# Performance work log

Measured on AMD Instinct MI355X. Metric: run time of the kernel, lower is better.

## Reference

```python
import jax, jax.numpy as jnp
import numpy as np

D, H = 256, 8
DH = D // H
NH, NL = 1024, 65536
EH, EL = 16384, 262144


def setup_inputs() -> dict:
    key = jax.random.key(0)
    ks = jax.random.split(key, 24)
    w = lambda i, s=0.05: jax.random.normal(ks[i], (D, D), jnp.float32) * s
    z = jnp.zeros((D,), jnp.float32)
    return {
        'high_emb_in': jax.random.normal(ks[0], (NH, D), jnp.float32),
        'low_emb_in': jax.random.normal(ks[1], (NL, D), jnp.float32),
        'high_edge_index': jax.random.randint(ks[2], (2, EH), 0, NH, jnp.int32),
        'low_edge_index': jax.random.randint(ks[3], (2, EL), 0, NL, jnp.int32),
        'low_batch': jnp.sort(jax.random.randint(ks[4], (NL,), 0, NH, jnp.int32)),
        'ln_g': jnp.ones((D,), jnp.float32), 'ln_b': z,
        'gin_eps': jnp.zeros((), jnp.float32), 'gin_w': w(5), 'gin_b': z,
        'mha_wq': w(6), 'mha_bq': z, 'mha_wk': w(7), 'mha_bk': z,
        'mha_wv': w(8), 'mha_bv': z, 'mha_wo': w(9), 'mha_bo': z,
        'tc_wq': w(10), 'tc_bq': z, 'tc_wk': w(11), 'tc_bk': z,
        'tc_wv': w(12), 'tc_bv': z, 'tc_wskip': w(13), 'tc_bskip': z,
        'chl_q': w(14), 'chl_k': w(15), 'chl_v': w(16),
        'clh_q': w(17), 'clh_k': w(18), 'clh_v': w(19),
    }


def _ln(x, g, b):
    m = x.mean(-1, keepdims=True)
    v = ((x - m) ** 2).mean(-1, keepdims=True)
    return (x - m) / jnp.sqrt(v + 1e-5) * g + b


def reference(high_emb_in, low_emb_in, ln_g, ln_b, gin_eps, gin_w, gin_b,
              mha_wq, mha_bq, mha_wk, mha_bk, mha_wv, mha_bv, mha_wo, mha_bo,
              tc_wq, tc_bq, tc_wk, tc_bk, tc_wv, tc_bv, tc_wskip, tc_bskip,
              chl_q, chl_k, chl_v, clh_q, clh_k, clh_v,
              high_edge_index, low_edge_index, low_batch):
    he = _ln(high_emb_in, ln_g, ln_b)
    le = _ln(low_emb_in, ln_g, ln_b)

    # --- GINConv(Linear) on high graph: Linear((1+eps)*x + sum_{j->i} x_j) ---
    hs, hd = high_edge_index[0], high_edge_index[1]
    agg = jax.ops.segment_sum(he[hs], hd, num_segments=NH)
    gin = ((1.0 + gin_eps) * he + agg) @ gin_w + gin_b

    # --- MultiheadAttention (unbatched self-attention over high nodes) ---
    q = (he @ mha_wq + mha_bq).reshape(NH, H, DH)
    k = (he @ mha_wk + mha_bk).reshape(NH, H, DH)
    v = (he @ mha_wv + mha_bv).reshape(NH, H, DH)
    logits = jnp.einsum('qhd,khd->hqk', q, k) * (1.0 / DH ** 0.5)
    attn = jax.nn.softmax(logits, axis=-1)
    mh = jnp.einsum('hqk,khd->qhd', attn, v).reshape(NH, D) @ mha_wo + mha_bo
    high = mh + gin

    # --- TransformerConv on low graph (concat heads + root skip) ---
    ls, lt = low_edge_index[0], low_edge_index[1]
    tq = (le @ tc_wq + tc_bq).reshape(NL, H, DH)
    tk = (le @ tc_wk + tc_bk).reshape(NL, H, DH)
    tv = (le @ tc_wv + tc_bv).reshape(NL, H, DH)
    lg = (tq[lt] * tk[ls]).sum(-1) * (1.0 / DH ** 0.5)  # [EL, H]
    mx = jax.ops.segment_max(lg, lt, num_segments=NL)
    p = jnp.exp(lg - mx[lt])
    den = jax.ops.segment_sum(p, lt, num_segments=NL)
    alpha = p / den[lt]
    msg = jax.ops.segment_sum(alpha[:, :, None] * tv[ls], lt, num_segments=NL)
    low = msg.reshape(NL, D) + le @ tc_wskip + tc_bskip

    # --- cross message passing ---
    cnt = jax.ops.segment_sum(jnp.ones((NL,), low.dtype), low_batch, num_segments=NH)
    xg = jax.ops.segment_sum(low, low_batch, num_segments=NH) / jnp.maximum(cnt, 1.0)[:, None]
    hpn = high[low_batch]
    sd = 1.0 / D ** 0.5
    w_hl = ((high @ chl_q) * (xg @ chl_k)).sum(1) * sd
    new_high = w_hl[:, None] * (high @ chl_v)
    w_lh = ((low @ clh_q) * (hpn @ clh_k)).sum(1) * sd
    new_low = w_lh[:, None] * (low @ clh_v)
    return (jax.nn.gelu(new_high, approximate=False),
            jax.nn.gelu(new_low, approximate=False))
```

## Files before the change

### kernel.cpp

```cpp
#include <hip/hip_runtime.h>
#include <math.h>

#define D 256
#define H 8
#define DH 32
#define NH 1024
#define NL 65536
#define EH 16384
#define EL 262144

typedef short bf16x8 __attribute__((ext_vector_type(8)));
typedef float f32x4 __attribute__((ext_vector_type(4)));

__device__ __forceinline__ float4 ld4(const float* p) { return *reinterpret_cast<const float4*>(p); }
__device__ __forceinline__ void st4(float* p, float4 v) { *reinterpret_cast<float4*>(p) = v; }
__device__ __forceinline__ float gelu_f(float x) { return 0.5f * x * (1.0f + erff(x * 0.70710678118654752f)); }
__device__ __forceinline__ ushort f2bf(float x) {
    union { float f; unsigned u; } v; v.f = x;
    unsigned r = v.u + 0x7FFF + ((v.u >> 16) & 1);
    return (ushort)(r >> 16);
}
__device__ __forceinline__ float bf2f(ushort u) {
    union { unsigned u; float f; } v; v.u = (unsigned)u << 16; return v.f;
}
__device__ __forceinline__ float4 bf4tof4(ushort4 u) {
    return make_float4(bf2f(u.x), bf2f(u.y), bf2f(u.z), bf2f(u.w));
}

__global__ __launch_bounds__(256) void ln_kernel(const float* __restrict__ hi, const float* __restrict__ lo,
                                                 const float* __restrict__ g, const float* __restrict__ b,
                                                 float* __restrict__ he, ushort* __restrict__ le16) {
    int row = blockIdx.x * 4 + (threadIdx.x >> 6);
    int lane = threadIdx.x & 63;
    const float* in = (row < NH) ? hi + (size_t)row * D : lo + (size_t)(row - NH) * D;
    float4 x = ld4(in + lane * 4);
    float s1 = x.x + x.y + x.z + x.w;
    float s2 = x.x * x.x + x.y * x.y + x.z * x.z + x.w * x.w;
    #pragma unroll
    for (int o = 32; o > 0; o >>= 1) { s1 += __shfl_xor(s1, o); s2 += __shfl_xor(s2, o); }
    float m = s1 * (1.0f / D);
    float var = s2 * (1.0f / D) - m * m;
    float rs = 1.0f / sqrtf(var + 1e-5f);
    float4 gg = ld4(g + lane * 4), bb = ld4(b + lane * 4);
    float4 y;
    y.x = (x.x - m) * rs * gg.x + bb.x;
    y.y = (x.y - m) * rs * gg.y + bb.y;
    y.z = (x.z - m) * rs * gg.z + bb.z;
    y.w = (x.w - m) * rs * gg.w + bb.w;
    if (row < NH) {
        st4(he + (size_t)row * D + lane * 4, y);
    } else {
        ushort4 u = make_ushort4(f2bf(y.x), f2bf(y.y), f2bf(y.z), f2bf(y.w));
        *reinterpret_cast<ushort4*>(le16 + (size_t)(row - NH) * D + lane * 4) = u;
    }
}

__global__ void concat_w(float* __restrict__ dst, const float* s0, const float* s1,
                         const float* s2, const float* s3, int nseg) {
    int total = 256 * nseg * 256;
    for (int idx = blockIdx.x * blockDim.x + threadIdx.x; idx < total; idx += gridDim.x * blockDim.x) {
        int ncol = nseg * 256;
        int r = idx / ncol, c = idx - r * ncol;
        int seg = c >> 8, cc = c & 255;
        const float* s = (seg == 0) ? s0 : (seg == 1) ? s1 : (seg == 2) ? s2 : s3;
        dst[idx] = s[r * 256 + cc];
    }
}
__global__ void concat_b(float* __restrict__ dst, const float* s0, const float* s1,
                         const float* s2, const float* s3, int nseg) {
    int idx = blockIdx.x * blockDim.x + threadIdx.x;
    if (idx < nseg * 256) {
        int seg = idx >> 8, cc = idx & 255;
        const float* s = (seg == 0) ? s0 : (seg == 1) ? s1 : (seg == 2) ? s2 : s3;
        dst[idx] = s[cc];
    }
}
__global__ __launch_bounds__(256) void concat_wT6(ushort* __restrict__ WlowT,
                                                  ushort* __restrict__ qT, ushort* __restrict__ vT,
                                                  const float* s18, const float* s20, const float* s22,
                                                  const float* s24, const float* s29, const float* s31) {
    int idx = blockIdx.x * 256 + threadIdx.x;
    int seg = idx >> 16, local = idx & 65535;
    int n = local >> 8, k = local & 255;
    const float* s; ushort* d; int off;
    switch (seg) {
        case 0: s = s18; d = WlowT; off = 0; break;
        case 1: s = s20; d = WlowT; off = 65536; break;
        case 2: s = s22; d = WlowT; off = 131072; break;
        case 3: s = s24; d = WlowT; off = 196608; break;
        case 4: s = s29; d = qT;    off = 0; break;
        default: s = s31; d = vT;   off = 0; break;
    }
    d[off + local] = f2bf(s[k * 256 + n]);
}

__global__ __launch_bounds__(256) void hcsr_count(const int* __restrict__ ei, int* __restrict__ counts) {
    int e = blockIdx.x * 256 + threadIdx.x;
    atomicAdd(&counts[ei[EH + e]], 1);
}
__global__ __launch_bounds__(256) void hscan(const int* __restrict__ cnt, int* __restrict__ rowptr) {
    __shared__ int s[256];
    int t = threadIdx.x;
    int v0 = cnt[t * 4], v1 = cnt[t * 4 + 1], v2 = cnt[t * 4 + 2], v3 = cnt[t * 4 + 3];
    int sum = v0 + v1 + v2 + v3;
    s[t] = sum;
    __syncthreads();
    for (int off = 1; off < 256; off <<= 1) {
        int v = (t >= off) ? s[t - off] : 0;
        __syncthreads();
        s[t] += v;
        __syncthreads();
    }
    int run = s[t] - sum;
    rowptr[t * 4] = run; run += v0;
    rowptr[t * 4 + 1] = run; run += v1;
    rowptr[t * 4 + 2] = run; run += v2;
    rowptr[t * 4 + 3] = run;
    if (t == 255) rowptr[NH] = EH;
}
__global__ __launch_bounds__(256) void hcsr_fill(const int* __restrict__ ei, const int* __restrict__ rowptr,
                                                 int* __restrict__ cursor, int* __restrict__ srcslot) {
    int e = blockIdx.x * 256 + threadIdx.x;
    int dst = ei[EH + e], src = ei[e];
    int pos = rowptr[dst] + atomicAdd(&cursor[dst], 1);
    srcslot[pos] = src;
}
__global__ __launch_bounds__(256) void gin_gather(const float* __restrict__ he, const int* __restrict__ rowptr,
                                                  const int* __restrict__ srcslot, const float* __restrict__ eps,
                                                  float* __restrict__ X) {
    int dst = blockIdx.x * 4 + (threadIdx.x >> 6);
    int lane = threadIdx.x & 63;
    float4 x = ld4(he + (size_t)dst * D + lane * 4);
    float e1 = 1.0f + eps[0];
    float4 acc = make_float4(e1 * x.x, e1 * x.y, e1 * x.z, e1 * x.w);
    int start = rowptr[dst], end = rowptr[dst + 1];
    for (int i = start; i < end; i++) {
        float4 v = ld4(he + (size_t)srcslot[i] * D + lane * 4);
        acc.x += v.x; acc.y += v.y; acc.z += v.z; acc.w += v.w;
    }
    st4(X + (size_t)dst * D + lane * 4, acc);
}

__global__ __launch_bounds__(256) void mm64(const float* __restrict__ A, int lda,
                                            const float* __restrict__ B, int ldb,
                                            const float* __restrict__ bias,
                                            const float* __restrict__ addC, int ldadd,
                                            float* __restrict__ C, int ldc) {
    __shared__ float As[16][64];
    __shared__ float Bs[16][64];
    int tid = threadIdx.x;
    int tx = tid & 15, ty = tid >> 4;
    int m0 = blockIdx.y * 64, n0 = blockIdx.x * 64;
    float acc[4][4];
    #pragma unroll
    for (int i = 0; i < 4; i++)
        #pragma unroll
        for (int j = 0; j < 4; j++) acc[i][j] = 0.0f;

    for (int k0 = 0; k0 < 256; k0 += 16) {
        {
            int row = tid >> 2, c4 = tid & 3;
            float4 a = ld4(A + (size_t)(m0 + row) * lda + k0 + c4 * 4);
            As[c4 * 4 + 0][row] = a.x; As[c4 * 4 + 1][row] = a.y;
            As[c4 * 4 + 2][row] = a.z; As[c4 * 4 + 3][row] = a.w;
        }
        {
            int row = tid >> 4, c4 = tid & 15;
            float4 b = ld4(B + (size_t)(k0 + row) * ldb + n0 + c4 * 4);
            st4(&Bs[row][c4 * 4], b);
        }
        __syncthreads();
        #pragma unroll
        for (int kk = 0; kk < 16; kk++) {
            float4 a4 = ld4(&As[kk][ty * 4]);
            float4 b4 = ld4(&Bs[kk][tx * 4]);
            float av[4] = {a4.x, a4.y, a4.z, a4.w};
            float bv[4] = {b4.x, b4.y, b4.z, b4.w};
            #pragma unroll
            for (int i = 0; i < 4; i++)
                #pragma unroll
                for (int j = 0; j < 4; j++) acc[i][j] += av[i] * bv[j];
        }
        __syncthreads();
    }
    float4 bj = bias ? ld4(bias + n0 + tx * 4) : make_float4(0.f, 0.f, 0.f, 0.f);
    #pragma unroll
    for (int i = 0; i < 4; i++) {
        size_t row = m0 + ty * 4 + i;
        float4 o = make_float4(acc[i][0] + bj.x, acc[i][1] + bj.y, acc[i][2] + bj.z, acc[i][3] + bj.w);
        if (addC) {
            float4 c = ld4(addC + row * ldadd + n0 + tx * 4);
            o.x += c.x; o.y += c.y; o.z += c.z; o.w += c.w;
        }
        st4(C + row * ldc + n0 + tx * 4, o);
    }
}

__global__ __launch_bounds__(256) void mm_bf16_o16(const ushort* __restrict__ A, int lda,
                                                   const ushort* __restrict__ BT,
                                                   const float* __restrict__ bias,
                                                   ushort* __restrict__ C, int ldc, int nbx) {
    __shared__ ushort As[128][40];
    __shared__ ushort Bs[128][40];
    int orig = blockIdx.x;
    int wg = (orig & 7) * (gridDim.x >> 3) + (orig >> 3);
    int m0 = (wg / nbx) * 128, n0 = (wg % nbx) * 128;
    int tid = threadIdx.x;
    int lane = tid & 63, wave = tid >> 6;
    int wm = wave >> 1, wn = wave & 1;
    int lrow = lane & 15, lgrp = lane >> 4;
    f32x4 acc[4][4];
    #pragma unroll
    for (int i = 0; i < 4; i++)
        #pragma unroll
        for (int j = 0; j < 4; j++) acc[i][j] = (f32x4){0.f, 0.f, 0.f, 0.f};

    int r0 = tid >> 2, q0 = tid & 3;
    int r1 = r0 + 64;
    for (int k0 = 0; k0 < 256; k0 += 32) {
        *(bf16x8*)&As[r0][q0 * 8] = *(const bf16x8*)&A[(size_t)(m0 + r0) * lda + k0 + q0 * 8];
        *(bf16x8*)&As[r1][q0 * 8] = *(const bf16x8*)&A[(size_t)(m0 + r1) * lda + k0 + q0 * 8];
        *(bf16x8*)&Bs[r0][q0 * 8] = *(const bf16x8*)&BT[(size_t)(n0 + r0) * 256 + k0 + q0 * 8];
        *(bf16x8*)&Bs[r1][q0 * 8] = *(const bf16x8*)&BT[(size_t)(n0 + r1) * 256 + k0 + q0 * 8];
        __syncthreads();
        bf16x8 af[4], bfr[4];
        #pragma unroll
        for (int f = 0; f < 4; f++) {
            af[f]  = *(const bf16x8*)&As[wm * 64 + f * 16 + lrow][lgrp * 8];
            bfr[f] = *(const bf16x8*)&Bs[wn * 64 + f * 16 + lrow][lgrp * 8];
        }
        #pragma unroll
        for (int i = 0; i < 4; i++)
            #pragma unroll
            for (int j = 0; j < 4; j++)
                acc[i][j] = __builtin_amdgcn_mfma_f32_16x16x32_bf16(af[i], bfr[j], acc[i][j], 0, 0, 0);
        __syncthreads();
    }
    #pragma unroll
    for (int i = 0; i < 4; i++) {
        #pragma unroll
        for (int j = 0; j < 4; j++) {
            int col = n0 + wn * 64 + j * 16 + lrow;
            float bb = bias ? bias[col] : 0.0f;
            #pragma unroll
            for (int r = 0; r < 4; r++) {
                int row = m0 + wm * 64 + i * 16 + lgrp * 4 + r;
                C[(size_t)row * ldc + col] = f2bf(acc[i][j][r] + bb);
            }
        }
    }
}

__global__ __launch_bounds__(64) void attn_part(const float* __restrict__ qkv, float* __restrict__ part) {
    __shared__ float ks[64][32];
    __shared__ float vs[64][32];
    int h = blockIdx.y, kc = blockIdx.z;
    int q0 = blockIdx.x * 64;
    int t = threadIdx.x;
    float qr[32];
    const float* qp = qkv + (size_t)(q0 + t) * 768 + h * 32;
    #pragma unroll
    for (int d = 0; d < 32; d += 4) {
        float4 x = ld4(qp + d);
        qr[d] = x.x; qr[d + 1] = x.y; qr[d + 2] = x.z; qr[d + 3] = x.w;
    }
    int kt = kc * 64;
    #pragma unroll
    for (int j = 0; j < 8; j++) {
        int f = j * 64 + t;
        int row = f >> 3, c4 = f & 7;
        float4 kx = ld4(qkv + (size_t)(kt + row) * 768 + 256 + h * 32 + c4 * 4);
        st4(&ks[row][c4 * 4], kx);
        float4 vx = ld4(qkv + (size_t)(kt + row) * 768 + 512 + h * 32 + c4 * 4);
        st4(&vs[row][c4 * 4], vx);
    }
    __syncthreads();
    float l = 0.0f, acc[32];
    #pragma unroll
    for (int d = 0; d < 32; d++) acc[d] = 0.0f;
    const float scale = 0.17677669529663687f;
    #pragma unroll 4
    for (int kk = 0; kk < 64; kk++) {
        const float4* kr = reinterpret_cast<const float4*>(&ks[kk][0]);
        float s = 0.0f;
        #pragma unroll
        for (int d4 = 0; d4 < 8; d4++) {
            float4 kv = kr[d4];
            s += qr[d4*4]*kv.x + qr[d4*4+1]*kv.y + qr[d4*4+2]*kv.z + qr[d4*4+3]*kv.w;
        }
        float pe = __expf(s * scale);
        l += pe;
        const float4* vr = reinterpret_cast<const float4*>(&vs[kk][0]);
        #pragma unroll
        for (int d4 = 0; d4 < 8; d4++) {
            float4 vv = vr[d4];
            acc[d4*4] += pe*vv.x; acc[d4*4+1] += pe*vv.y; acc[d4*4+2] += pe*vv.z; acc[d4*4+3] += pe*vv.w;
        }
    }
    int q = q0 + t;
    size_t base = ((size_t)(h * 16 + kc) * 33) * 1024 + q;
    #pragma unroll
    for (int d = 0; d < 32; d++) part[base + (size_t)d * 1024] = acc[d];
    part[base + (size_t)32 * 1024] = l;
}

__global__ __launch_bounds__(64) void attn_combine(const float* __restrict__ part, float* __restrict__ out) {
    int h = blockIdx.y;
    int q = blockIdx.x * 64 + threadIdx.x;
    float acc[32], l = 0.0f;
    #pragma unroll
    for (int d = 0; d < 32; d++) acc[d] = 0.0f;
    for (int kc = 0; kc < 16; kc++) {
        size_t base = ((size_t)(h * 16 + kc) * 33) * 1024 + q;
        #pragma unroll
        for (int d = 0; d < 32; d++) acc[d] += part[base + (size_t)d * 1024];
        l += part[base + (size_t)32 * 1024];
    }
    float inv = 1.0f / l;
    float* op = out + (size_t)q * 256 + h * 32;
    #pragma unroll
    for (int d = 0; d < 32; d += 4)
        st4(op + d, make_float4(acc[d]*inv, acc[d+1]*inv, acc[d+2]*inv, acc[d+3]*inv));
}

__global__ __launch_bounds__(256) void csr_count(const int* __restrict__ ei, int* __restrict__ counts) {
    int e = blockIdx.x * 256 + threadIdx.x;
    atomicAdd(&counts[ei[EL + e]], 1);
}
__global__ __launch_bounds__(256) void scan_a(const int* __restrict__ counts, int* __restrict__ rowptr,
                                              int* __restrict__ bsum) {
    __shared__ int s[256];
    int t = threadIdx.x;
    int i = blockIdx.x * 256 + t;
    int c = counts[i];
    s[t] = c;
    __syncthreads();
    for (int off = 1; off < 256; off <<= 1) {
        int v = (t >= off) ? s[t - off] : 0;
        __syncthreads();
        s[t] += v;
        __syncthreads();
    }
    rowptr[i] = s[t] - c;
    if (t == 255) bsum[blockIdx.x] = s[255];
}
__global__ __launch_bounds__(256) void scan_b(int* __restrict__ bsum) {
    __shared__ int s[256];
    int t = threadIdx.x;
    int c = bsum[t];
    s[t] = c;
    __syncthreads();
    for (int off = 1; off < 256; off <<= 1) {
        int v = (t >= off) ? s[t - off] : 0;
        __syncthreads();
        s[t] += v;
        __syncthreads();
    }
    bsum[t] = s[t] - c;
}
__global__ __launch_bounds__(256) void scan_c(int* __restrict__ rowptr, const int* __restrict__ bsum) {
    int i = blockIdx.x * 256 + threadIdx.x;
    rowptr[i] += bsum[blockIdx.x];
    if (i == 0) rowptr[NL] = EL;
}
__global__ __launch_bounds__(256) void csr_fill(const int* __restrict__ ei, const int* __restrict__ rowptr,
                                                int* __restrict__ cursor, int* __restrict__ srcslot) {
    int e = blockIdx.x * 256 + threadIdx.x;
    int dst = ei[EL + e], src = ei[e];
    int pos = rowptr[dst] + atomicAdd(&cursor[dst], 1);
    srcslot[pos] = src;
}

__global__ __launch_bounds__(256) void edge_g1(const ushort* __restrict__ panel, const int* __restrict__ rowptr,
                                               const int* __restrict__ srcslot,
                                               float* __restrict__ p, float* __restrict__ den) {
    int dst = blockIdx.x * 4 + (threadIdx.x >> 6);
    int lane = threadIdx.x & 63, hh = lane >> 3;
    int start = rowptr[dst], end = rowptr[dst + 1];
    float4 q4 = bf4tof4(*(const ushort4*)&panel[(size_t)dst * 1024 + lane * 4]);
    float dl = 0.0f;
    for (int i = start; i < end; i++) {
        int src = srcslot[i];
        float4 k4 = bf4tof4(*(const ushort4*)&panel[(size_t)src * 1024 + 256 + lane * 4]);
        float s = q4.x * k4.x + q4.y * k4.y + q4.z * k4.z + q4.w * k4.w;
        s += __shfl_xor(s, 1); s += __shfl_xor(s, 2); s += __shfl_xor(s, 4);
        float pe = __expf(s * 0.17677669529663687f);
        dl += pe;
        if ((lane & 7) == 0) p[(size_t)i * 8 + hh] = pe;
    }
    if ((lane & 7) == 0) den[(size_t)dst * 8 + hh] = dl;
}

__global__ __launch_bounds__(256) void edge_g2(ushort* panel, const int* __restrict__ rowptr,
                                               const int* __restrict__ srcslot,
                                               const float* __restrict__ p, const float* __restrict__ den) {
    int dst = blockIdx.x * 4 + (threadIdx.x >> 6);
    int lane = threadIdx.x & 63, hh = lane >> 3;
    int start = rowptr[dst], end = rowptr[dst + 1];
    float dl = den[(size_t)dst * 8 + hh];
    float invd = (dl != 0.0f) ? 1.0f / dl : 0.0f;
    float4 acc = make_float4(0.f, 0.f, 0.f, 0.f);
    for (int i = start; i < end; i++) {
        int src = srcslot[i];
        float a = p[(size_t)i * 8 + hh] * invd;
        float4 v4 = bf4tof4(*(const ushort4*)&panel[(size_t)src * 1024 + 512 + lane * 4]);
        acc.x += a * v4.x; acc.y += a * v4.y; acc.z += a * v4.z; acc.w += a * v4.w;
    }
    ushort* op = panel + (size_t)dst * 1024 + 768 + lane * 4;
    float4 sk = bf4tof4(*(const ushort4*)op);
    ushort4 u = make_ushort4(f2bf(acc.x + sk.x), f2bf(acc.y + sk.y), f2bf(acc.z + sk.z), f2bf(acc.w + sk.w));
    *reinterpret_cast<ushort4*>(op) = u;
}

__global__ __launch_bounds__(256) void xg_kernel(const ushort* __restrict__ panel,
                                                 const int* __restrict__ batch, float* __restrict__ xg) {
    int i = blockIdx.x;
    int d = threadIdx.x;
    int lo = 0, hi = NL;
    while (lo < hi) { int mid = (lo + hi) >> 1; if (batch[mid] < i) lo = mid + 1; else hi = mid; }
    int start = lo;
    hi = NL;
    while (lo < hi) { int mid = (lo + hi) >> 1; if (batch[mid] < i + 1) lo = mid + 1; else hi = mid; }
    int end = lo;
    float s = 0.0f;
    for (int r = start; r < end; r++) s += bf2f(panel[(size_t)r * 1024 + 768 + d]);
    xg[i * 256 + d] = s / fmaxf((float)(end - start), 1.0f);
}

__global__ __launch_bounds__(256) void out_high_kernel(const float* __restrict__ highX,
                                                       const float* __restrict__ xk, float* __restrict__ out) {
    int i = blockIdx.x * 4 + (threadIdx.x >> 6);
    int lane = threadIdx.x & 63;
    float4 hq = ld4(highX + (size_t)i * 768 + lane * 4);
    float4 xkv = ld4(xk + (size_t)i * 256 + lane * 4);
    float s = hq.x * xkv.x + hq.y * xkv.y + hq.z * xkv.z + hq.w * xkv.w;
    #pragma unroll
    for (int o = 32; o > 0; o >>= 1) s += __shfl_xor(s, o);
    float w = s * 0.0625f;
    float4 hv = ld4(highX + (size_t)i * 768 + 256 + lane * 4);
    st4(out + (size_t)i * 256 + lane * 4,
        make_float4(gelu_f(w * hv.x), gelu_f(w * hv.y), gelu_f(w * hv.z), gelu_f(w * hv.w)));
}

__global__ __launch_bounds__(256) void out_low_kernel(const ushort* __restrict__ panel,
                                                      const float* __restrict__ highX,
                                                      const int* __restrict__ batch, float* __restrict__ out) {
    int i = blockIdx.x * 4 + (threadIdx.x >> 6);
    int lane = threadIdx.x & 63;
    int b = batch[i];
    float4 lq = bf4tof4(*(const ushort4*)&panel[(size_t)i * 1024 + lane * 4]);
    float4 hk = ld4(highX + (size_t)b * 768 + 512 + lane * 4);
    float s = lq.x * hk.x + lq.y * hk.y + lq.z * hk.z + lq.w * hk.w;
    #pragma unroll
    for (int o = 32; o > 0; o >>= 1) s += __shfl_xor(s, o);
    float w = s * 0.0625f;
    float4 lv = bf4tof4(*(const ushort4*)&panel[(size_t)i * 1024 + 256 + lane * 4]);
    st4(out + (size_t)i * 256 + lane * 4,
        make_float4(gelu_f(w * lv.x), gelu_f(w * lv.y), gelu_f(w * lv.z), gelu_f(w * lv.w)));
}

extern "C" void kernel_launch(void* const* d_in, const int* in_sizes, int n_in,
                              void* d_out, int out_size, void* d_ws, size_t ws_size,
                              hipStream_t stream) {
    const float* high_in = (const float*)d_in[0];
    const float* low_in  = (const float*)d_in[1];
    const int*   hei     = (const int*)d_in[2];
    const int*   lei     = (const int*)d_in[3];
    const int*   batch   = (const int*)d_in[4];
    const float* ln_g    = (const float*)d_in[5];
    const float* ln_b    = (const float*)d_in[6];
    const float* gin_eps = (const float*)d_in[7];
    const float* gin_w   = (const float*)d_in[8];
    const float* gin_b   = (const float*)d_in[9];
    const float* mha_wo  = (const float*)d_in[16];
    const float* mha_bo  = (const float*)d_in[17];
    const float* chl_k   = (const float*)d_in[27];

    float* out = (float*)d_out;
    ushort* le16 = (ushort*)d_out;

    float* ws    = (float*)d_ws;
    ushort* panel = (ushort*)ws;
    float* pbuf  = ws + (size_t)NL * 512;
    float* den   = pbuf + 4325376;
    float* xg    = den + (size_t)NL * 8;
    float* he    = xg + (size_t)NH * 256;
    float* aggx  = he + (size_t)NH * 256;
    float* gin   = aggx + (size_t)NH * 256;
    float* qkv   = gin + (size_t)NH * 256;
    float* attno = qkv + (size_t)NH * 768;
    float* high  = attno + (size_t)NH * 256;
    float* highX = high + (size_t)NH * 256;
    float* xk    = highX + (size_t)NH * 768;
    float* Wmha  = xk + (size_t)NH * 256;
    float* bmha  = Wmha + 256 * 768;
    float* Whx   = bmha + 768;
    float* bqk   = Whx + 256 * 768;
    ushort* WlowT = (ushort*)(bqk + 1024);
    ushort* clhqT = WlowT + 1024 * 256;
    ushort* clhvT = clhqT + 256 * 256;
    int* rowptr  = (int*)(clhvT + 256 * 256);
    int* cursor  = rowptr + NL + 1;
    int* bsum    = cursor + NL;
    int* srcslot = bsum + 256;
    int* hcnt    = srcslot + EL;
    int* hrow    = hcnt + NH;
    int* hsrc    = hrow + NH + 1;

    concat_w<<<768, 256, 0, stream>>>(Wmha, (const float*)d_in[10], (const float*)d_in[12], (const float*)d_in[14], nullptr, 3);
    concat_b<<<3, 256, 0, stream>>>(bmha, (const float*)d_in[11], (const float*)d_in[13], (const float*)d_in[15], nullptr, 3);
    concat_w<<<768, 256, 0, stream>>>(Whx, (const float*)d_in[26], (const float*)d_in[28], (const float*)d_in[30], nullptr, 3);
    concat_b<<<4, 256, 0, stream>>>(bqk, (const float*)d_in[19], (const float*)d_in[21], (const float*)d_in[23], (const float*)d_in[25], 4);
    concat_wT6<<<1536, 256, 0, stream>>>(WlowT, clhqT, clhvT,
                                         (const float*)d_in[18], (const float*)d_in[20], (const float*)d_in[22],
                                         (const float*)d_in[24], (const float*)d_in[29], (const float*)d_in[31]);

    hipMemsetAsync(cursor, 0, NL * sizeof(int), stream);
    csr_count<<<EL / 256, 256, 0, stream>>>(lei, cursor);
    scan_a<<<256, 256, 0, stream>>>(cursor, rowptr, bsum);
    scan_b<<<1, 256, 0, stream>>>(bsum);
    scan_c<<<256, 256, 0, stream>>>(rowptr, bsum);
    hipMemsetAsync(cursor, 0, NL * sizeof(int), stream);
    csr_fill<<<EL / 256, 256, 0, stream>>>(lei, rowptr, cursor, srcslot);

    hipMemsetAsync(hcnt, 0, NH * sizeof(int), stream);
    hcsr_count<<<EH / 256, 256, 0, stream>>>(hei, hcnt);
    hscan<<<1, 256, 0, stream>>>(hcnt, hrow);
    hipMemsetAsync(hcnt, 0, NH * sizeof(int), stream);
    hcsr_fill<<<EH / 256, 256, 0, stream>>>(hei, hrow, hcnt, hsrc);

    ln_kernel<<<(NH + NL) / 4, 256, 0, stream>>>(high_in, low_in, ln_g, ln_b, he, le16);

    gin_gather<<<NH / 4, 256, 0, stream>>>(he, hrow, hsrc, gin_eps, aggx);
    mm64<<<dim3(4, 16), 256, 0, stream>>>(aggx, 256, gin_w, 256, gin_b, nullptr, 0, gin, 256);

    mm64<<<dim3(12, 16), 256, 0, stream>>>(he, 256, Wmha, 768, bmha, nullptr, 0, qkv, 768);
    attn_part<<<dim3(16, H, 16), 64, 0, stream>>>(qkv, pbuf);
    attn_combine<<<dim3(16, H), 64, 0, stream>>>(pbuf, attno);
    mm64<<<dim3(4, 16), 256, 0, stream>>>(attno, 256, mha_wo, 256, mha_bo, gin, 256, high, 256);

    mm_bf16_o16<<<4096, 256, 0, stream>>>(le16, 256, WlowT, bqk, panel, 1024, 8);

    edge_g1<<<NL / 4, 256, 0, stream>>>(panel, rowptr, srcslot, pbuf, den);

    edge_g2<<<NL / 4, 256, 0, stream>>>(panel, rowptr, srcslot, pbuf, den);

    xg_kernel<<<NH, 256, 0, stream>>>(panel, batch, xg);

    mm64<<<dim3(12, 16), 256, 0, stream>>>(high, 256, Whx, 768, nullptr, nullptr, 0, highX, 768);
    mm64<<<dim3(4, 16), 256, 0, stream>>>(xg, 256, chl_k, 256, nullptr, nullptr, 0, xk, 256);
    out_high_kernel<<<NH / 4, 256, 0, stream>>>(highX, xk, out);

    mm_bf16_o16<<<2048, 256, 0, stream>>>(panel + 768, 1024, clhqT, nullptr, panel, 1024, 4);

    out_low_kernel<<<NL / 4, 256, 0, stream>>>(panel, highX, batch, out + (size_t)NH * 256);
}
```

Baseline: 657.2 us.

## Fuse edge softmax passes into one kernel and use direct global-to-LDS loads

Merges the two graph-transformer edge kernels into a single pass. Each wave reads the adjacent K and V slices of a source row with one 16-byte load, computes the unnormalized exp weights, accumulates weighted V, and normalizes once at the end, so the p and den buffers and the second gather over edges are no longer needed. The bf16 GEMM now stages tiles with global_load_lds straight into unpadded LDS instead of going through registers. Dropping the padding may raise LDS bank conflicts when fragments are read. The fused kernel also drops max-subtraction from the softmax, as the kernel it replaces already did.

```diff
diff --git a/kernel.cpp b/kernel.cpp
--- a/kernel.cpp
+++ b/kernel.cpp
@@ -25,6 +25,10 @@
 }
 __device__ __forceinline__ float4 bf4tof4(ushort4 u) {
     return make_float4(bf2f(u.x), bf2f(u.y), bf2f(u.z), bf2f(u.w));
+}
+__device__ __forceinline__ void gload16(const ushort* g, ushort* l) {
+    __builtin_amdgcn_global_load_lds((const __attribute__((address_space(1))) void*)g,
+                                     (__attribute__((address_space(3))) void*)l, 16, 0, 0);
 }
 
 __global__ __launch_bounds__(256) void ln_kernel(const float* __restrict__ hi, const float* __restrict__ lo,
@@ -200,8 +204,8 @@
                                                    const ushort* __restrict__ BT,
                                                    const float* __restrict__ bias,
                                                    ushort* __restrict__ C, int ldc, int nbx) {
-    __shared__ ushort As[128][40];
-    __shared__ ushort Bs[128][40];
+    __shared__ ushort As[128][32];
+    __shared__ ushort Bs[128][32];
     int orig = blockIdx.x;
     int wg = (orig & 7) * (gridDim.x >> 3) + (orig >> 3);
     int m0 = (wg / nbx) * 128, n0 = (wg % nbx) * 128;
@@ -209,19 +213,19 @@
     int lane = tid & 63, wave = tid >> 6;
     int wm = wave >> 1, wn = wave & 1;
     int lrow = lane & 15, lgrp = lane >> 4;
+    int srow = wave * 16 + (lane >> 2);
+    int scq  = (lane & 3) * 8;
     f32x4 acc[4][4];
     #pragma unroll
     for (int i = 0; i < 4; i++)
         #pragma unroll
         for (int j = 0; j < 4; j++) acc[i][j] = (f32x4){0.f, 0.f, 0.f, 0.f};
 
-    int r0 = tid >> 2, q0 = tid & 3;
-    int r1 = r0 + 64;
     for (int k0 = 0; k0 < 256; k0 += 32) {
-        *(bf16x8*)&As[r0][q0 * 8] = *(const bf16x8*)&A[(size_t)(m0 + r0) * lda + k0 + q0 * 8];
-        *(bf16x8*)&As[r1][q0 * 8] = *(const bf16x8*)&A[(size_t)(m0 + r1) * lda + k0 + q0 * 8];
-        *(bf16x8*)&Bs[r0][q0 * 8] = *(const bf16x8*)&BT[(size_t)(n0 + r0) * 256 + k0 + q0 * 8];
-        *(bf16x8*)&Bs[r1][q0 * 8] = *(const bf16x8*)&BT[(size_t)(n0 + r1) * 256 + k0 + q0 * 8];
+        gload16(&A[(size_t)(m0 + srow) * lda + k0 + scq],        &As[wave * 16][0]);
+        gload16(&A[(size_t)(m0 + 64 + srow) * lda + k0 + scq],   &As[64 + wave * 16][0]);
+        gload16(&BT[(size_t)(n0 + srow) * 256 + k0 + scq],       &Bs[wave * 16][0]);
+        gload16(&BT[(size_t)(n0 + 64 + srow) * 256 + k0 + scq],  &Bs[64 + wave * 16][0]);
         __syncthreads();
         bf16x8 af[4], bfr[4];
         #pragma unroll
@@ -371,45 +375,49 @@
     srcslot[pos] = src;
 }
 
-__global__ __launch_bounds__(256) void edge_g1(const ushort* __restrict__ panel, const int* __restrict__ rowptr,
-                                               const int* __restrict__ srcslot,
-                                               float* __restrict__ p, float* __restrict__ den) {
+__global__ __launch_bounds__(256) void edge_fused(ushort* panel, const int* __restrict__ rowptr,
+                                                  const int* __restrict__ srcslot) {
     int dst = blockIdx.x * 4 + (threadIdx.x >> 6);
-    int lane = threadIdx.x & 63, hh = lane >> 3;
+    int lane = threadIdx.x & 63;
     int start = rowptr[dst], end = rowptr[dst + 1];
-    float4 q4 = bf4tof4(*(const ushort4*)&panel[(size_t)dst * 1024 + lane * 4]);
-    float dl = 0.0f;
+    float q[8];
+    {
+        bf16x8 q8 = *(const bf16x8*)&panel[(size_t)dst * 1024 + (lane & 31) * 8];
+        #pragma unroll
+        for (int j = 0; j < 8; j++) q[j] = bf2f(((ushort*)&q8)[j]);
+    }
+    float acc[8];
+    #pragma unroll
+    for (int j = 0; j < 8; j++) acc[j] = 0.0f;
+    float dsum = 0.0f;
+    const float scale = 0.17677669529663687f;
     for (int i = start; i < end; i++) {
         int src = srcslot[i];
-        float4 k4 = bf4tof4(*(const ushort4*)&panel[(size_t)src * 1024 + 256 + lane * 4]);
-        float s = q4.x * k4.x + q4.y * k4.y + q4.z * k4.z + q4.w * k4.w;
-        s += __shfl_xor(s, 1); s += __shfl_xor(s, 2); s += __shfl_xor(s, 4);
-        float pe = __expf(s * 0.17677669529663687f);
-        dl += pe;
-        if ((lane & 7) == 0) p[(size_t)i * 8 + hh] = pe;
-    }
-    if ((lane & 7) == 0) den[(size_t)dst * 8 + hh] = dl;
-}
-
-__global__ __launch_bounds__(256) void edge_g2(ushort* panel, const int* __restrict__ rowptr,
-                                               const int* __restrict__ srcslot,
-                                               const float* __restrict__ p, const float* __restrict__ den) {
-    int dst = blockIdx.x * 4 + (threadIdx.x >> 6);
-    int lane = threadIdx.x & 63, hh = lane >> 3;
-    int start = rowptr[dst], end = rowptr[dst + 1];
-    float dl = den[(size_t)dst * 8 + hh];
-    float invd = (dl != 0.0f) ? 1.0f / dl : 0.0f;
-    float4 acc = make_float4(0.f, 0.f, 0.f, 0.f);
-    for (int i = start; i < end; i++) {
-        int src = srcslot[i];
-        float a = p[(size_t)i * 8 + hh] * invd;
-        float4 v4 = bf4tof4(*(const ushort4*)&panel[(size_t)src * 1024 + 512 + lane * 4]);
-        acc.x += a * v4.x; acc.y += a * v4.y; acc.z += a * v4.z; acc.w += a * v4.w;
-    }
-    ushort* op = panel + (size_t)dst * 1024 + 768 + lane * 4;
-    float4 sk = bf4tof4(*(const ushort4*)op);
-    ushort4 u = make_ushort4(f2bf(acc.x + sk.x), f2bf(acc.y + sk.y), f2bf(acc.z + sk.z), f2bf(acc.w + sk.w));
-    *reinterpret_cast<ushort4*>(op) = u;
+        bf16x8 kv8 = *(const bf16x8*)&panel[(size_t)src * 1024 + 256 + lane * 8];
+        float x[8];
+        #pragma unroll
+        for (int j = 0; j < 8; j++) x[j] = bf2f(((ushort*)&kv8)[j]);
+        float s = q[0]*x[0] + q[1]*x[1] + q[2]*x[2] + q[3]*x[3]
+                + q[4]*x[4] + q[5]*x[5] + q[6]*x[6] + q[7]*x[7];
+        s += __shfl_xor(s, 1);
+        s += __shfl_xor(s, 2);
+        float pe = __expf(s * scale);
+        dsum += pe;
+        float pv = __shfl_xor(pe, 32);
+        #pragma unroll
+        for (int j = 0; j < 8; j++) acc[j] += pv * x[j];
+    }
+    float dv = __shfl_xor(dsum, 32);
+    float invd = (dv != 0.0f) ? 1.0f / dv : 0.0f;
+    if (lane >= 32) {
+        ushort* op = &panel[(size_t)dst * 1024 + 768 + (size_t)(lane - 32) * 8];
+        bf16x8 sk8 = *(const bf16x8*)op;
+        bf16x8 o;
+        #pragma unroll
+        for (int j = 0; j < 8; j++)
+            ((ushort*)&o)[j] = f2bf(acc[j] * invd + bf2f(((ushort*)&sk8)[j]));
+        *(bf16x8*)op = o;
+    }
 }
 
 __global__ __launch_bounds__(256) void xg_kernel(const ushort* __restrict__ panel,
@@ -541,9 +549,7 @@
 
     mm_bf16_o16<<<4096, 256, 0, stream>>>(le16, 256, WlowT, bqk, panel, 1024, 8);
 
-    edge_g1<<<NL / 4, 256, 0, stream>>>(panel, rowptr, srcslot, pbuf, den);
-
-    edge_g2<<<NL / 4, 256, 0, stream>>>(panel, rowptr, srcslot, pbuf, den);
+    edge_fused<<<NL / 4, 256, 0, stream>>>(panel, rowptr, srcslot);
 
     xg_kernel<<<NH, 256, 0, stream>>>(panel, batch, xg);
 
```

Measured after the change: 619.3 us. -5.8%, faster.
